# Performance work log

Hardware: AMD Instinct MI355X
Metric: run time of the kernel (lower is better)

The kernel has to match this reference:

```python
import jax, jax.numpy as jnp
import numpy as np

HIDDEN, KEY_DIM, VALUE_DIM = 1024, 64, 64
B, T = 4, 4096


def setup_inputs() -> dict:
    key = jax.random.key(0)
    ks = jax.random.split(key, 9)
    s = 0.02
    return {
        "y_all": jax.random.normal(ks[0], (B, T, HIDDEN), dtype=jnp.float32),
        # torch nn.Linear weights: (out_features, in_features)
        "Wq": jax.random.normal(ks[1], (KEY_DIM, HIDDEN), dtype=jnp.float32) * s,
        "bq": jax.random.normal(ks[2], (KEY_DIM,), dtype=jnp.float32) * s,
        "Wk": jax.random.normal(ks[3], (KEY_DIM, HIDDEN), dtype=jnp.float32) * s,
        "bk": jax.random.normal(ks[4], (KEY_DIM,), dtype=jnp.float32) * s,
        "Wv": jax.random.normal(ks[5], (VALUE_DIM, HIDDEN), dtype=jnp.float32) * s,
        "bv": jax.random.normal(ks[6], (VALUE_DIM,), dtype=jnp.float32) * s,
        "Wo": jax.random.normal(ks[7], (HIDDEN, VALUE_DIM), dtype=jnp.float32) * s,
        "bo": jax.random.normal(ks[8], (HIDDEN,), dtype=jnp.float32) * s,
    }


def reference(y_all, Wq, bq, Wk, bk, Wv, bv, Wo, bo):
    # The original per-timestep loop is exactly causal self-attention:
    # query at position i attends over positions 0..i.
    q = jnp.einsum("bth,kh->btk", y_all, Wq) + bq          # (B,T,Dk)
    k = jnp.einsum("bth,kh->btk", y_all, Wk) + bk          # (B,T,Dk)
    v = jnp.einsum("bth,vh->btv", y_all, Wv) + bv          # (B,T,Dv)
    scale = jnp.asarray(KEY_DIM, q.dtype) ** 0.5
    scores = jnp.einsum("bqk,btk->bqt", q / scale, k)      # (B,T,T)
    t = scores.shape[-1]
    causal = jnp.tril(jnp.ones((t, t), dtype=bool))
    scores = jnp.where(causal, scores, jnp.asarray(-jnp.inf, scores.dtype))
    weights = jax.nn.softmax(scores, axis=-1)
    ctx = jnp.einsum("bqt,btv->bqv", weights, v)           # (B,T,Dv)
    out = jnp.einsum("bqv,hv->bqh", ctx, Wo) + bo          # (B,T,H)
    return out
```

## Files before the change

### kernel.cpp

```cpp
#include <hip/hip_runtime.h>


typedef __attribute__((ext_vector_type(4)))  float f32x4;
typedef __attribute__((ext_vector_type(16))) float f32x16;
typedef __attribute__((ext_vector_type(8)))  short s16x8;
typedef __attribute__((ext_vector_type(4)))  short s16x4;

#define DEV static __device__ __forceinline__

static constexpr int TT = 4096;
static constexpr int HH = 1024;
static constexpr int DD = 64;
static constexpr float MNEG = -3.0e38f;

DEV unsigned short f2bf(float f) {
  union { float f; unsigned int u; } v; v.f = f;
  unsigned int r = v.u + 0x7FFFu + ((v.u >> 16) & 1u);
  return (unsigned short)(r >> 16);
}

DEV float bf2f(unsigned short u) {
  union { unsigned int u; float f; } v; v.u = ((unsigned int)u) << 16;
  return v.f;
}

DEV unsigned int pk2(float lo, float hi) {
  return (unsigned int)f2bf(lo) | ((unsigned int)f2bf(hi) << 16);
}

DEV s16x8 mk8(unsigned int w0, unsigned int w1, unsigned int w2, unsigned int w3) {
  union { unsigned int u[4]; s16x8 v; } c;
  c.u[0] = w0; c.u[1] = w1; c.u[2] = w2; c.u[3] = w3; return c.v;
}

DEV int swzA(int row) { return ((row & 7) << 4); }
DEV int swzK(int row) { return ((row & 7) << 4) ^ ((row & 8) << 3); }

__global__ void prep_kernel(const float* __restrict__ Wq, const float* __restrict__ Wk,
                            const float* __restrict__ Wv, const float* __restrict__ Wo,
                            unsigned short* __restrict__ Wall,
                            unsigned short* __restrict__ Wo_b)
{
  int i = blockIdx.x * blockDim.x + threadIdx.x;
  int stride = gridDim.x * blockDim.x;
  const int n1 = 64 * HH;
  for (int idx = i; idx < 3 * n1; idx += stride) {
    float v = idx < n1 ? Wq[idx] : (idx < 2 * n1 ? Wk[idx - n1] : Wv[idx - 2 * n1]);
    Wall[idx] = f2bf(v);
  }
  for (int idx = i; idx < HH * DD; idx += stride) {
    int hcol = idx >> 6, d = idx & 63;
    size_t off = (size_t)(hcol >> 4) * 1024 + (d >> 5) * 512 + (hcol & 15) * 32
               + ((d >> 3) & 3) * 8 + (d & 7);
    Wo_b[off] = f2bf(Wo[idx]);
  }
}

__global__ __launch_bounds__(256, 2) void qkv_kernel(
    const float* __restrict__ y, const unsigned short* __restrict__ Wall,
    const float* __restrict__ bq, const float* __restrict__ bk,
    const float* __restrict__ bv,
    unsigned short* __restrict__ q_ws, unsigned short* __restrict__ k_ws,
    unsigned short* __restrict__ vT_ws)
{
  __shared__ unsigned short ylds[2][32 * 64];
  __shared__ unsigned short wlds[2][192 * 64];
  const int t = threadIdx.x;
  const int wv = t >> 6, lane = t & 63, g = lane >> 4, c = lane & 15;
  const int row0 = blockIdx.x * 32;
  const int bb = row0 >> 12;
  const int tb = row0 & 4095;
  const int yrow = t >> 3, ycol0 = (t & 7) * 8;

  f32x4 acc[2][3];
#pragma unroll
  for (int m = 0; m < 2; ++m)
#pragma unroll
    for (int i = 0; i < 3; ++i)
#pragma unroll
      for (int e = 0; e < 4; ++e) acc[m][i][e] = 0.0f;

  f32x4 yr[2];
  s16x8 wr[6];

  auto load_tiles = [&](int kb) {
    const float* src = y + (size_t)(row0 + yrow) * HH + kb * 64 + ycol0;
    yr[0] = *(const f32x4*)(src);
    yr[1] = *(const f32x4*)(src + 4);
#pragma unroll
    for (int ii = 0; ii < 6; ++ii) {
      int ch = t + ii * 256;
      int rw = ch >> 3, c0 = (ch & 7) * 8;
      wr[ii] = *(const s16x8*)(Wall + (size_t)rw * HH + kb * 64 + c0);
    }
  };
  auto write_tiles = [&](int buf) {
    s16x8 h0;
#pragma unroll
    for (int e = 0; e < 4; ++e) {
      h0[e]     = (short)f2bf(yr[0][e]);
      h0[e + 4] = (short)f2bf(yr[1][e]);
    }
    int byte0 = yrow * 128 + ycol0 * 2;
    *(s16x8*)((char*)ylds[buf] + (byte0 ^ swzA(yrow))) = h0;
#pragma unroll
    for (int ii = 0; ii < 6; ++ii) {
      int ch = t + ii * 256;
      int rw = ch >> 3, c0 = (ch & 7) * 8;
      int byte = rw * 128 + c0 * 2;
      *(s16x8*)((char*)wlds[buf] + (byte ^ swzA(rw))) = wr[ii];
    }
  };

  load_tiles(0);
  write_tiles(0);
  __syncthreads();
  for (int kb = 0; kb < 16; ++kb) {
    int buf = kb & 1;
    if (kb < 15) load_tiles(kb + 1);
#pragma unroll
    for (int kk = 0; kk < 2; ++kk) {
      s16x8 a[2], bfr[3];
#pragma unroll
      for (int m = 0; m < 2; ++m) {
        int ra = 16 * m + c;
        a[m] = *(const s16x8*)((char*)ylds[buf] +
                 ((ra * 128 + (kk * 32 + 8 * g) * 2) ^ swzA(ra)));
      }
#pragma unroll
      for (int i = 0; i < 3; ++i) {
        int rb = 16 * (3 * wv + i) + c;
        bfr[i] = *(const s16x8*)((char*)wlds[buf] +
                   ((rb * 128 + (kk * 32 + 8 * g) * 2) ^ swzA(rb)));
      }
#pragma unroll
      for (int m = 0; m < 2; ++m)
#pragma unroll
        for (int i = 0; i < 3; ++i)
          acc[m][i] = __builtin_amdgcn_mfma_f32_16x16x32_bf16(a[m], bfr[i], acc[m][i], 0, 0, 0);
    }
    __syncthreads();
    if (kb < 15) { write_tiles((kb + 1) & 1); __syncthreads(); }
  }

  unsigned short* elds = &wlds[0][0];
  const float qsc = 1.4426950408889634f / 8.0f;
#pragma unroll
  for (int m = 0; m < 2; ++m)
#pragma unroll
    for (int i = 0; i < 3; ++i) {
      int nt = 3 * wv + i;
      int sec = nt >> 2;
      int dcol = (nt & 3) * 16 + c;
      float bias = sec == 0 ? bq[dcol] : (sec == 1 ? bk[dcol] : bv[dcol]);
#pragma unroll
      for (int i2 = 0; i2 < 4; ++i2) {
        int rl = 16 * m + 4 * g + i2;
        float val = acc[m][i][i2] + bias;
        if (sec == 0) val *= qsc;
        if (sec < 2) elds[sec * 2048 + rl * 64 + dcol] = f2bf(val);
        else         elds[4096 + dcol * 32 + rl]       = f2bf(val);
      }
    }
  __syncthreads();
  {
    int trow = t >> 3, d0 = (t & 7) * 8;
    s16x8 vq = *(const s16x8*)(elds + trow * 64 + d0);
    s16x8 vk = *(const s16x8*)(elds + 2048 + trow * 64 + d0);
    size_t offqk = (size_t)bb * (TT * DD) + (size_t)(tb >> 5) * 2048
                 + (d0 >> 4) * 512 + trow * 16 + (d0 & 15);
    *(s16x8*)(q_ws + offqk) = vq;
    *(s16x8*)(k_ws + offqk) = vk;
    int d = t >> 2, tq = (t & 3) * 8;
    s16x8 vvv = *(const s16x8*)(elds + 4096 + d * 32 + tq);
    int tg = tb + tq;
    size_t offv = (size_t)bb * (DD * TT) + (size_t)(tg >> 6) * 4096
                + (d >> 5) * 2048 + ((tg >> 4) & 3) * 512 + (d & 31) * 16 + (tg & 15);
    *(s16x8*)(vT_ws + offv) = vvv;
  }
}

__global__ __launch_bounds__(512, 4) void attn_kernel(
    const unsigned short* __restrict__ q_ws, const unsigned short* __restrict__ k_ws,
    const unsigned short* __restrict__ vT_ws, const unsigned short* __restrict__ Wo_b,
    const float* __restrict__ bo, float* __restrict__ out)
{
  __shared__ char smem[32256];
  unsigned short* obuf = (unsigned short*)smem;
  float* mstat = (float*)(smem + 28672);
  unsigned short* clds = (unsigned short*)smem;
  const int t = threadIdx.x, wp = t >> 6, lane = t & 63;
  const int qcol = lane & 31, h = lane >> 5;
  const int b = blockIdx.x & 3;
  const int u = blockIdx.x >> 2;
  const int j32 = (u < 64) ? (126 - 2 * u) : (2 * (u - 64) + 1);
  const int q0 = j32 * 32;
  const int L = j32 >> 1;
  const size_t base  = (size_t)b * TT * DD;
  const size_t vbase = (size_t)b * DD * TT;
  const int g = lane >> 4, c = lane & 15;
  const int lchunk = (lane & 31) * 16 + (lane >> 5) * 8;

  s16x8 qf[4];
  {
    const unsigned short* qp = q_ws + base + (size_t)j32 * 2048;
#pragma unroll
    for (int kk = 0; kk < 4; ++kk) qf[kk] = *(const s16x8*)(qp + kk * 512 + lchunk);
  }
  f32x16 o[2];
#pragma unroll
  for (int mt = 0; mt < 2; ++mt)
#pragma unroll
    for (int rg = 0; rg < 16; ++rg) o[mt][rg] = 0.0f;
  float m_run = MNEG, l_run = 0.0f;

  for (int kt = wp; kt <= L; kt += 8) {
    const int kv0 = kt * 64;
    s16x8 kf[2][4];
#pragma unroll
    for (int mt = 0; mt < 2; ++mt)
#pragma unroll
      for (int kk = 0; kk < 4; ++kk)
        kf[mt][kk] = *(const s16x8*)(k_ws + base +
                       (size_t)(2 * kt + mt) * 2048 + kk * 512 + lchunk);
    f32x16 s[2];
#pragma unroll
    for (int mt = 0; mt < 2; ++mt)
#pragma unroll
      for (int rg = 0; rg < 16; ++rg) s[mt][rg] = 0.0f;
    __builtin_amdgcn_s_setprio(1);
#pragma unroll
    for (int kk = 0; kk < 4; ++kk)
#pragma unroll
      for (int mt = 0; mt < 2; ++mt)
        s[mt] = __builtin_amdgcn_mfma_f32_32x32x16_bf16(kf[mt][kk], qf[kk], s[mt], 0, 0, 0);
    __builtin_amdgcn_s_setprio(0);
    s16x8 vf[2][4];
#pragma unroll
    for (int mt = 0; mt < 2; ++mt)
#pragma unroll
      for (int ks = 0; ks < 4; ++ks)
        vf[mt][ks] = *(const s16x8*)(vT_ws + vbase +
                       (size_t)kt * 4096 + mt * 2048 + ks * 512 + lchunk);
    if (kt == L) {
      int qq = q0 + qcol;
#pragma unroll
      for (int mt = 0; mt < 2; ++mt)
#pragma unroll
        for (int rg = 0; rg < 16; ++rg) {
          int kvabs = kv0 + 32 * mt + (rg & 3) + 8 * (rg >> 2) + 4 * h;
          if (kvabs > qq) s[mt][rg] = MNEG;
        }
    }
    float mx[16];
#pragma unroll
    for (int e = 0; e < 16; ++e) mx[e] = fmaxf(s[0][e], s[1][e]);
#pragma unroll
    for (int st = 8; st >= 1; st >>= 1)
#pragma unroll
      for (int e = 0; e < 8; ++e) if (e < st) mx[e] = fmaxf(mx[e], mx[e + st]);
    float pm = fmaxf(mx[0], __shfl_xor(mx[0], 32));
    float m_new;
    if (__all(pm - m_run <= 8.0f)) {
      m_new = m_run;
    } else {
      m_new = fmaxf(m_run, pm);
      float alpha = exp2f(m_run - m_new);
      l_run *= alpha;
#pragma unroll
      for (int mt = 0; mt < 2; ++mt)
#pragma unroll
        for (int rg = 0; rg < 16; ++rg) o[mt][rg] *= alpha;
      m_run = m_new;
    }
#pragma unroll
    for (int mt = 0; mt < 2; ++mt)
#pragma unroll
      for (int rg = 0; rg < 16; ++rg) s[mt][rg] = exp2f(s[mt][rg] - m_new);
    float sm[16];
#pragma unroll
    for (int e = 0; e < 16; ++e) sm[e] = s[0][e] + s[1][e];
#pragma unroll
    for (int st = 8; st >= 1; st >>= 1)
#pragma unroll
      for (int e = 0; e < 8; ++e) if (e < st) sm[e] += sm[e + st];
    float rowsum = sm[0] + __shfl_xor(sm[0], 32);
    l_run += rowsum;
    s16x8 pf[4];
#pragma unroll
    for (int mt = 0; mt < 2; ++mt) {
      unsigned int a0 = pk2(s[mt][0],  s[mt][1]);
      unsigned int a1 = pk2(s[mt][2],  s[mt][3]);
      unsigned int b0 = pk2(s[mt][4],  s[mt][5]);
      unsigned int b1 = pk2(s[mt][6],  s[mt][7]);
      unsigned int c0 = pk2(s[mt][8],  s[mt][9]);
      unsigned int c1 = pk2(s[mt][10], s[mt][11]);
      unsigned int d0 = pk2(s[mt][12], s[mt][13]);
      unsigned int d1 = pk2(s[mt][14], s[mt][15]);
      unsigned int t0 = __shfl_xor(h ? a0 : b0, 32);
      unsigned int t1 = __shfl_xor(h ? a1 : b1, 32);
      unsigned int t2 = __shfl_xor(h ? c0 : d0, 32);
      unsigned int t3 = __shfl_xor(h ? c1 : d1, 32);
      pf[2 * mt]     = mk8(h ? t0 : a0, h ? t1 : a1, h ? b0 : t0, h ? b1 : t1);
      pf[2 * mt + 1] = mk8(h ? t2 : c0, h ? t3 : c1, h ? d0 : t2, h ? d1 : t3);
    }
    __builtin_amdgcn_s_setprio(1);
#pragma unroll
    for (int ks = 0; ks < 4; ++ks)
#pragma unroll
      for (int mt = 0; mt < 2; ++mt)
        o[mt] = __builtin_amdgcn_mfma_f32_32x32x16_bf16(vf[mt][ks], pf[ks], o[mt], 0, 0, 0);
    __builtin_amdgcn_s_setprio(0);
  }

  if (wp != 0) {
    unsigned short* ob = obuf + (wp - 1) * 2048;
#pragma unroll
    for (int mt = 0; mt < 2; ++mt)
#pragma unroll
      for (int rg = 0; rg < 16; ++rg)
        ob[(mt * 16 + rg) * 64 + lane] = f2bf(o[mt][rg]);
    mstat[(wp - 1) * 128 + lane] = m_run;
    mstat[(wp - 1) * 128 + 64 + lane] = l_run;
  }
  __syncthreads();
  if (wp == 0) {
    float mB[7], lB[7];
    float mS = m_run;
#pragma unroll
    for (int i = 0; i < 7; ++i) {
      mB[i] = mstat[i * 128 + lane];
      lB[i] = mstat[i * 128 + 64 + lane];
      mS = fmaxf(mS, mB[i]);
    }
    float f0 = exp2f(m_run - mS);
    float fi[7];
    float l_tot = l_run * f0;
#pragma unroll
    for (int i = 0; i < 7; ++i) { fi[i] = exp2f(mB[i] - mS); l_tot += lB[i] * fi[i]; }
    float inv = 1.0f / l_tot;
#pragma unroll
    for (int mt = 0; mt < 2; ++mt)
#pragma unroll
      for (int rg = 0; rg < 16; ++rg) {
        float val = o[mt][rg] * f0;
#pragma unroll
        for (int i = 0; i < 7; ++i)
          val += bf2f(obuf[i * 2048 + (mt * 16 + rg) * 64 + lane]) * fi[i];
        o[mt][rg] = val * inv;
      }
  }
  __syncthreads();
  if (wp == 0) {
#pragma unroll
    for (int mt = 0; mt < 2; ++mt) {
#pragma unroll
      for (int rgq = 0; rgq < 4; ++rgq) {
        s16x4 pb;
#pragma unroll
        for (int e = 0; e < 4; ++e) pb[e] = (short)f2bf(o[mt][4 * rgq + e]);
        int d0 = 32 * mt + 8 * rgq + 4 * h;
        int byte = qcol * 128 + d0 * 2;
        *(s16x4*)((char*)clds + (byte ^ swzK(qcol))) = pb;
      }
    }
  }
  __syncthreads();

  s16x8 afr[2][2];
#pragma unroll
  for (int mt = 0; mt < 2; ++mt)
#pragma unroll
    for (int kk = 0; kk < 2; ++kk) {
      int ra = 16 * mt + c;
      afr[mt][kk] = *(const s16x8*)((char*)clds +
                      ((ra * 128 + (32 * kk + 8 * g) * 2) ^ swzK(ra)));
    }
  const int wchunk = (lane & 15) * 32 + (lane >> 4) * 8;
  const size_t orow0 = (size_t)(b * TT + q0);
#pragma unroll 4
  for (int nt = 0; nt < 8; ++nt) {
    int nt16 = wp * 8 + nt;
    int col = nt16 * 16 + c;
    s16x8 bfr[2];
#pragma unroll
    for (int kk = 0; kk < 2; ++kk)
      bfr[kk] = *(const s16x8*)(Wo_b + (size_t)nt16 * 1024 + kk * 512 + wchunk);
    f32x4 acc4[2];
#pragma unroll
    for (int mt = 0; mt < 2; ++mt)
#pragma unroll
      for (int e = 0; e < 4; ++e) acc4[mt][e] = 0.0f;
#pragma unroll
    for (int kk = 0; kk < 2; ++kk)
#pragma unroll
      for (int mt = 0; mt < 2; ++mt)
        acc4[mt] = __builtin_amdgcn_mfma_f32_16x16x32_bf16(afr[mt][kk], bfr[kk],
                                                           acc4[mt], 0, 0, 0);
    float bias = bo[col];
#pragma unroll
    for (int mt = 0; mt < 2; ++mt)
#pragma unroll
      for (int i = 0; i < 4; ++i) {
        size_t row = orow0 + 16 * mt + 4 * g + i;
        out[row * HH + col] = acc4[mt][i] + bias;
      }
  }
}

extern "C" void kernel_launch(void* const* d_in, const int* in_sizes, int n_in,
                              void* d_out, int out_size, void* d_ws, size_t ws_size,
                              hipStream_t stream)
{
  const float* y  = (const float*)d_in[0];
  const float* Wq = (const float*)d_in[1];
  const float* bq = (const float*)d_in[2];
  const float* Wk = (const float*)d_in[3];
  const float* bk = (const float*)d_in[4];
  const float* Wv = (const float*)d_in[5];
  const float* bv = (const float*)d_in[6];
  const float* Wo = (const float*)d_in[7];
  const float* bo = (const float*)d_in[8];
  float* out = (float*)d_out;
  char* ws = (char*)d_ws;
  unsigned short* Wall  = (unsigned short*)(ws);
  unsigned short* Wo_b  = (unsigned short*)(ws + 393216);
  unsigned short* q_ws  = (unsigned short*)(ws + 524288);
  unsigned short* k_ws  = (unsigned short*)(ws + 524288 + 2097152);
  unsigned short* vT_ws = (unsigned short*)(ws + 524288 + 2 * 2097152);

  prep_kernel<<<dim3(256), dim3(256), 0, stream>>>(Wq, Wk, Wv, Wo, Wall, Wo_b);
  qkv_kernel<<<dim3(512), dim3(256), 0, stream>>>(y, Wall, bq, bk, bv, q_ws, k_ws, vT_ws);
  attn_kernel<<<dim3(512), dim3(512), 0, stream>>>(q_ws, k_ws, vT_ws, Wo_b, bo, out);
}
```

Baseline: 67.29 us.

## Halve attention block to four waves, use hardware bf16 packing and permlane swaps

The attention kernel drops from 8 to 4 waves per block, so each wave walks more key tiles and the cross-wave merge reads 3 partials instead of 7. The partial outputs are kept in fp32 in LDS rather than bf16, and the normalize step is folded into the bf16 write to drop one barrier. Software bf16 rounding plus shuffle/select is replaced by v_cvt_pk_bf16_f32 and v_permlane32_swap, and the block ordering for causal load balance is reversed. Fewer waves per block lowers parallelism within each query tile and lengthens the serial KV loop per wave.

Measured after the change: 58.29 us (median of 2 runs). -13.4%, faster.

```diff
diff --git a/kernel.cpp b/kernel.cpp
--- a/kernel.cpp
+++ b/kernel.cpp
@@ -19,13 +19,10 @@
   return (unsigned short)(r >> 16);
 }
 
-DEV float bf2f(unsigned short u) {
-  union { unsigned int u; float f; } v; v.u = ((unsigned int)u) << 16;
-  return v.f;
-}
-
-DEV unsigned int pk2(float lo, float hi) {
-  return (unsigned int)f2bf(lo) | ((unsigned int)f2bf(hi) << 16);
+DEV unsigned int cvtpk(float lo, float hi) {
+  unsigned int r;
+  asm("v_cvt_pk_bf16_f32 %0, %1, %2" : "=v"(r) : "v"(lo), "v"(hi));
+  return r;
 }
 
 DEV s16x8 mk8(unsigned int w0, unsigned int w1, unsigned int w2, unsigned int w3) {
@@ -180,20 +177,19 @@
   }
 }
 
-__global__ __launch_bounds__(512, 4) void attn_kernel(
+__global__ __launch_bounds__(256, 2) void attn_kernel(
     const unsigned short* __restrict__ q_ws, const unsigned short* __restrict__ k_ws,
     const unsigned short* __restrict__ vT_ws, const unsigned short* __restrict__ Wo_b,
     const float* __restrict__ bo, float* __restrict__ out)
 {
-  __shared__ char smem[32256];
-  unsigned short* obuf = (unsigned short*)smem;
-  float* mstat = (float*)(smem + 28672);
-  unsigned short* clds = (unsigned short*)smem;
-  const int t = threadIdx.x, wp = t >> 6, lane = t & 63;
+  __shared__ float obuf[3 * 2048];
+  __shared__ float mstat[3 * 128];
+  __shared__ unsigned short clds[32 * 64];
+  const int t = threadIdx.x, wv = t >> 6, lane = t & 63;
   const int qcol = lane & 31, h = lane >> 5;
   const int b = blockIdx.x & 3;
-  const int u = blockIdx.x >> 2;
-  const int j32 = (u < 64) ? (126 - 2 * u) : (2 * (u - 64) + 1);
+  const int jslot = blockIdx.x >> 2;
+  const int j32 = (jslot < 64) ? (2 * jslot) : (127 - 2 * (jslot - 64));
   const int q0 = j32 * 32;
   const int L = j32 >> 1;
   const size_t base  = (size_t)b * TT * DD;
@@ -214,7 +210,7 @@
     for (int rg = 0; rg < 16; ++rg) o[mt][rg] = 0.0f;
   float m_run = MNEG, l_run = 0.0f;
 
-  for (int kt = wp; kt <= L; kt += 8) {
+  for (int kt = wv; kt <= L; kt += 4) {
     const int kv0 = kt * 64;
     s16x8 kf[2][4];
 #pragma unroll
@@ -289,20 +285,20 @@
     s16x8 pf[4];
 #pragma unroll
     for (int mt = 0; mt < 2; ++mt) {
-      unsigned int a0 = pk2(s[mt][0],  s[mt][1]);
-      unsigned int a1 = pk2(s[mt][2],  s[mt][3]);
-      unsigned int b0 = pk2(s[mt][4],  s[mt][5]);
-      unsigned int b1 = pk2(s[mt][6],  s[mt][7]);
-      unsigned int c0 = pk2(s[mt][8],  s[mt][9]);
-      unsigned int c1 = pk2(s[mt][10], s[mt][11]);
-      unsigned int d0 = pk2(s[mt][12], s[mt][13]);
-      unsigned int d1 = pk2(s[mt][14], s[mt][15]);
-      unsigned int t0 = __shfl_xor(h ? a0 : b0, 32);
-      unsigned int t1 = __shfl_xor(h ? a1 : b1, 32);
-      unsigned int t2 = __shfl_xor(h ? c0 : d0, 32);
-      unsigned int t3 = __shfl_xor(h ? c1 : d1, 32);
-      pf[2 * mt]     = mk8(h ? t0 : a0, h ? t1 : a1, h ? b0 : t0, h ? b1 : t1);
-      pf[2 * mt + 1] = mk8(h ? t2 : c0, h ? t3 : c1, h ? d0 : t2, h ? d1 : t3);
+      unsigned int a0 = cvtpk(s[mt][0],  s[mt][1]);
+      unsigned int a1 = cvtpk(s[mt][2],  s[mt][3]);
+      unsigned int b0 = cvtpk(s[mt][4],  s[mt][5]);
+      unsigned int b1 = cvtpk(s[mt][6],  s[mt][7]);
+      unsigned int c0 = cvtpk(s[mt][8],  s[mt][9]);
+      unsigned int c1 = cvtpk(s[mt][10], s[mt][11]);
+      unsigned int d0 = cvtpk(s[mt][12], s[mt][13]);
+      unsigned int d1 = cvtpk(s[mt][14], s[mt][15]);
+      asm("v_permlane32_swap_b32 %0, %1" : "+v"(a0), "+v"(b0));
+      asm("v_permlane32_swap_b32 %0, %1" : "+v"(a1), "+v"(b1));
+      asm("v_permlane32_swap_b32 %0, %1" : "+v"(c0), "+v"(d0));
+      asm("v_permlane32_swap_b32 %0, %1" : "+v"(c1), "+v"(d1));
+      pf[2 * mt]     = mk8(a0, a1, b0, b1);
+      pf[2 * mt + 1] = mk8(c0, c1, d0, d1);
     }
     __builtin_amdgcn_s_setprio(1);
 #pragma unroll
@@ -313,52 +309,45 @@
     __builtin_amdgcn_s_setprio(0);
   }
 
-  if (wp != 0) {
-    unsigned short* ob = obuf + (wp - 1) * 2048;
+  if (wv != 0) {
 #pragma unroll
     for (int mt = 0; mt < 2; ++mt)
 #pragma unroll
       for (int rg = 0; rg < 16; ++rg)
-        ob[(mt * 16 + rg) * 64 + lane] = f2bf(o[mt][rg]);
-    mstat[(wp - 1) * 128 + lane] = m_run;
-    mstat[(wp - 1) * 128 + 64 + lane] = l_run;
+        obuf[(wv - 1) * 2048 + (mt * 16 + rg) * 64 + lane] = o[mt][rg];
+    mstat[(wv - 1) * 128 + lane] = m_run;
+    mstat[(wv - 1) * 128 + 64 + lane] = l_run;
   }
   __syncthreads();
-  if (wp == 0) {
-    float mB[7], lB[7];
+  if (wv == 0) {
+    float mB[3], lB[3];
     float mS = m_run;
 #pragma unroll
-    for (int i = 0; i < 7; ++i) {
+    for (int i = 0; i < 3; ++i) {
       mB[i] = mstat[i * 128 + lane];
       lB[i] = mstat[i * 128 + 64 + lane];
       mS = fmaxf(mS, mB[i]);
     }
     float f0 = exp2f(m_run - mS);
-    float fi[7];
+    float fi[3];
     float l_tot = l_run * f0;
 #pragma unroll
-    for (int i = 0; i < 7; ++i) { fi[i] = exp2f(mB[i] - mS); l_tot += lB[i] * fi[i]; }
+    for (int i = 0; i < 3; ++i) { fi[i] = exp2f(mB[i] - mS); l_tot += lB[i] * fi[i]; }
     float inv = 1.0f / l_tot;
-#pragma unroll
-    for (int mt = 0; mt < 2; ++mt)
-#pragma unroll
-      for (int rg = 0; rg < 16; ++rg) {
-        float val = o[mt][rg] * f0;
-#pragma unroll
-        for (int i = 0; i < 7; ++i)
-          val += bf2f(obuf[i * 2048 + (mt * 16 + rg) * 64 + lane]) * fi[i];
-        o[mt][rg] = val * inv;
-      }
-  }
-  __syncthreads();
-  if (wp == 0) {
 #pragma unroll
     for (int mt = 0; mt < 2; ++mt) {
 #pragma unroll
       for (int rgq = 0; rgq < 4; ++rgq) {
         s16x4 pb;
 #pragma unroll
-        for (int e = 0; e < 4; ++e) pb[e] = (short)f2bf(o[mt][4 * rgq + e]);
+        for (int e = 0; e < 4; ++e) {
+          int rg = 4 * rgq + e;
+          float val = o[mt][rg] * f0;
+#pragma unroll
+          for (int i = 0; i < 3; ++i)
+            val += obuf[i * 2048 + (mt * 16 + rg) * 64 + lane] * fi[i];
+          pb[e] = (short)f2bf(val * inv);
+        }
         int d0 = 32 * mt + 8 * rgq + 4 * h;
         int byte = qcol * 128 + d0 * 2;
         *(s16x4*)((char*)clds + (byte ^ swzK(qcol))) = pb;
@@ -379,13 +368,13 @@
   const int wchunk = (lane & 15) * 32 + (lane >> 4) * 8;
   const size_t orow0 = (size_t)(b * TT + q0);
 #pragma unroll 4
-  for (int nt = 0; nt < 8; ++nt) {
-    int nt16 = wp * 8 + nt;
-    int col = nt16 * 16 + c;
+  for (int nt = 0; nt < 16; ++nt) {
+    int col = wv * 256 + 16 * nt + c;
     s16x8 bfr[2];
 #pragma unroll
     for (int kk = 0; kk < 2; ++kk)
-      bfr[kk] = *(const s16x8*)(Wo_b + (size_t)nt16 * 1024 + kk * 512 + wchunk);
+      bfr[kk] = *(const s16x8*)(Wo_b + (size_t)(wv * 16 + nt) * 1024
+                                + kk * 512 + wchunk);
     f32x4 acc4[2];
 #pragma unroll
     for (int mt = 0; mt < 2; ++mt)
@@ -431,5 +420,5 @@
 
   prep_kernel<<<dim3(256), dim3(256), 0, stream>>>(Wq, Wk, Wv, Wo, Wall, Wo_b);
   qkv_kernel<<<dim3(512), dim3(256), 0, stream>>>(y, Wall, bq, bk, bv, q_ws, k_ws, vT_ws);
-  attn_kernel<<<dim3(512), dim3(512), 0, stream>>>(q_ws, k_ws, vT_ws, Wo_b, bo, out);
-}
+  attn_kernel<<<dim3(512), dim3(256), 0, stream>>>(q_ws, k_ws, vT_ws, Wo_b, bo, out);
+}
```
